# Optimization experiments

Measured on AMD Instinct MI355X. Metric: run time of the kernel, lower is better.

## Reference

```python
import jax, jax.numpy as jnp
import numpy as np

DIM = 1024
HID = 512
N_EXPERTS = 16
TOP_K = 4


def setup_inputs() -> dict:
    key = jax.random.key(0)
    ks = jax.random.split(key, 8)
    s = 0.02
    x = jax.random.normal(ks[0], (2, 1024, DIM), dtype=jnp.float32)
    gate_w = jax.random.normal(ks[1], (N_EXPERTS, DIM), dtype=jnp.float32) * s
    # stacked expert weights (nn.Linear stores [out, in]; we keep [E, out, in])
    w1 = jax.random.normal(ks[2], (N_EXPERTS, HID, DIM), dtype=jnp.float32) * s
    w3 = jax.random.normal(ks[3], (N_EXPERTS, HID, DIM), dtype=jnp.float32) * s
    w2 = jax.random.normal(ks[4], (N_EXPERTS, DIM, HID), dtype=jnp.float32) * s
    sw1 = jax.random.normal(ks[5], (HID, DIM), dtype=jnp.float32) * s
    sw3 = jax.random.normal(ks[6], (HID, DIM), dtype=jnp.float32) * s
    sw2 = jax.random.normal(ks[7], (DIM, HID), dtype=jnp.float32) * s
    return {"x": x, "gate_w": gate_w, "w1": w1, "w3": w3, "w2": w2,
            "sw1": sw1, "sw3": sw3, "sw2": sw2}


def reference(x, gate_w, w1, w3, w2, sw1, sw3, sw2):
    bsz, seq_len, dim = x.shape
    xf = x.reshape(-1, dim)                              # [T, d]
    T = xf.shape[0]

    # router: softmax -> top-k -> renormalize
    probs = jax.nn.softmax(xf @ gate_w.T, axis=-1)       # [T, E]
    top_w, top_idx = jax.lax.top_k(probs, TOP_K)         # [T, K]
    top_w = top_w / jnp.sum(top_w, axis=-1, keepdims=True)

    # combine weights as dense [T, E] (zero for unselected experts);
    # weighted dense per-expert compute is mathematically identical to the
    # gather/scatter loop since unselected experts get weight 0.
    rows = jnp.arange(T)[:, None]
    combine = jnp.zeros((T, N_EXPERTS), dtype=xf.dtype).at[rows, top_idx].set(top_w)

    h1 = jnp.einsum('td,ehd->teh', xf, w1)               # [T, E, h]
    h3 = jnp.einsum('td,ehd->teh', xf, w3)
    act = jax.nn.silu(h1) * h3
    eout = jnp.einsum('teh,edh->ted', act, w2)           # [T, E, d]
    moe_out = jnp.einsum('ted,te->td', eout, combine)    # [T, d]

    shared = (jax.nn.silu(xf @ sw1.T) * (xf @ sw3.T)) @ sw2.T
    return (moe_out + shared).reshape(bsz, seq_len, dim)
```

## Files before the change

### kernel.cpp

```cpp
#include <hip/hip_runtime.h>

#define DIM   1024
#define HID   512
#define NEXP  16
#define TOPK  4
#define SLOTS 5
#define PITCH 72
#define TPE   16

typedef unsigned short u16;
typedef unsigned int   u32;
typedef short bf16x8 __attribute__((ext_vector_type(8)));
typedef float f32x4  __attribute__((ext_vector_type(4)));

__device__ __forceinline__ float bf2f(u16 u) {
    union { u32 i; float f; } v; v.i = ((u32)u) << 16; return v.f;
}
__device__ __forceinline__ u16 f2bf(float f) {
    union { float f; u32 i; } v; v.f = f;
    u32 lsb = (v.i >> 16) & 1u;
    v.i += 0x7fffu + lsb;
    return (u16)(v.i >> 16);
}
__device__ __forceinline__ uint4 pack8(float4 a, float4 b) {
    uint4 r;
    r.x = (u32)f2bf(a.x) | ((u32)f2bf(a.y) << 16);
    r.y = (u32)f2bf(a.z) | ((u32)f2bf(a.w) << 16);
    r.z = (u32)f2bf(b.x) | ((u32)f2bf(b.y) << 16);
    r.w = (u32)f2bf(b.z) | ((u32)f2bf(b.w) << 16);
    return r;
}

#define CW ((size_t)NEXP * HID * DIM / 8)
#define CS ((size_t)HID * DIM / 8)
#define SEG_B0 (CW)
#define SEG_B1 (SEG_B0 + CS)
#define SEG_B2 (SEG_B1 + CW)
#define SEG_B3 (SEG_B2 + CS)
#define SEG_B4 (SEG_B3 + CW)
#define SEG_B5 (SEG_B4 + CS)

__global__ __launch_bounds__(256) void moe_prep(
    const float* __restrict__ x,    const float* __restrict__ gate,
    const float* __restrict__ w1,   const float* __restrict__ w3,
    const float* __restrict__ w2,   const float* __restrict__ sw1,
    const float* __restrict__ sw3,  const float* __restrict__ sw2,
    u16* __restrict__ dst,
    int* __restrict__ counts, u32* __restrict__ pairs,
    float* __restrict__ wslot, int T)
{
    const int blk = blockIdx.x;
    const int tid = threadIdx.x;
    if (blk >= T) {
        const size_t base = (size_t)(blk - T) * 512 + tid;
        const size_t totC = SEG_B5 + ((size_t)T << 7);
#pragma unroll
        for (int h = 0; h < 2; ++h) {
            const size_t c = base + (size_t)h * 256;
            if (c >= totC) break;
            const float* src; size_t loc;
            if      (c < SEG_B0) { src = w1;  loc = c; }
            else if (c < SEG_B1) { src = sw1; loc = c - SEG_B0; }
            else if (c < SEG_B2) { src = w3;  loc = c - SEG_B1; }
            else if (c < SEG_B3) { src = sw3; loc = c - SEG_B2; }
            else if (c < SEG_B4) { src = w2;  loc = c - SEG_B3; }
            else if (c < SEG_B5) { src = sw2; loc = c - SEG_B4; }
            else                 { src = x;   loc = c - SEG_B5; }
            float4 a = ((const float4*)src)[loc * 2];
            float4 b = ((const float4*)src)[loc * 2 + 1];
            ((uint4*)dst)[c] = pack8(a, b);
        }
        return;
    }
    const int t    = blk;
    const int lane = tid & 63;
    const int wv   = tid >> 6;
    const float* xrow = x + (size_t)t * DIM;
    float xr[16];
#pragma unroll
    for (int j = 0; j < 16; ++j) xr[j] = xrow[lane + 64 * j];

    __shared__ float slog[NEXP];
#pragma unroll
    for (int i = 0; i < 4; ++i) {
        const int e = wv * 4 + i;
        const float* g = gate + (size_t)e * DIM;
        float s = 0.f;
#pragma unroll
        for (int j = 0; j < 16; ++j) s += xr[j] * g[lane + 64 * j];
#pragma unroll
        for (int off = 32; off > 0; off >>= 1) s += __shfl_xor(s, off);
        if (lane == 0) slog[e] = s;
    }
    __syncthreads();
    if (wv != 0) return;

    float v[NEXP];
#pragma unroll
    for (int e = 0; e < NEXP; ++e) v[e] = slog[e];
    int idx[TOPK]; float lv[TOPK];
#pragma unroll
    for (int r = 0; r < TOPK; ++r) {
        int be = 0; float bv = v[0];
        for (int e = 1; e < NEXP; ++e) { if (v[e] > bv) { bv = v[e]; be = e; } }
        idx[r] = be; lv[r] = bv; v[be] = -3.0e38f;
    }
    float wk[TOPK]; float wsum = 0.f;
#pragma unroll
    for (int r = 0; r < TOPK; ++r) { wk[r] = __expf(lv[r] - lv[0]); wsum += wk[r]; }
#pragma unroll
    for (int r = 0; r < TOPK; ++r) wk[r] /= wsum;

    if (lane < TOPK) {
        int e = idx[lane];
        int slot = atomicAdd(&counts[e], 1);
        if (slot < T) pairs[(size_t)e * T + slot] = ((u32)t << 3) | (u32)lane;
        wslot[t * SLOTS + lane] = wk[lane];
    } else if (lane == TOPK) {
        pairs[(size_t)NEXP * T + t] = ((u32)t << 3) | 4u;
        wslot[t * SLOTS + 4] = 1.0f;
    }
}

__global__ __launch_bounds__(256) void moe_gemm1(
    const u16* __restrict__ xb,
    const u16* __restrict__ w1c, const u16* __restrict__ w3c,
    const u32* __restrict__ pairs, const int* __restrict__ counts,
    u16* __restrict__ act, int T)
{
    const int ytile = blockIdx.y;
    const int e     = ytile % (NEXP + 1);
    const int ti    = ytile / (NEXP + 1);
    const int r0    = ti << 7;
    const int n0    = blockIdx.x * 128;
    const int cnt = (e == NEXP) ? T : min(max(counts[e], 0), T);
    if (r0 >= cnt) return;
    const int nv = min(128, cnt - r0);

    const u16* W1 = w1c + (size_t)e * HID * DIM;
    const u16* W3 = w3c + (size_t)e * HID * DIM;

    __shared__ __align__(16) u16 sA [128 * PITCH];
    __shared__ __align__(16) u16 sB1[128 * PITCH];
    __shared__ __align__(16) u16 sB3[128 * PITCH];
    __shared__ u32 sEnt[128];

    const int tid = threadIdx.x;
    if (tid < 128) {
        u32 ent = (tid < nv) ? pairs[(size_t)e * T + r0 + tid] : 0u;
        u32 tk = ent >> 3, sl = ent & 7u;
        if (tk >= (u32)T) tk = 0;
        if (sl >= SLOTS)  sl = 0;
        sEnt[tid] = (tk << 3) | sl;
    }
    __syncthreads();

    const int ar = tid >> 1;
    const int ac = (tid & 1) * 32;
    const u16* xrow  = xb + (size_t)(sEnt[ar] >> 3) * DIM;
    const u16* b1row = W1 + (size_t)(n0 + ar) * DIM;
    const u16* b3row = W3 + (size_t)(n0 + ar) * DIM;

    const int wv   = tid >> 6;
    const int lane = tid & 63;
    const int l15  = lane & 15;
    const int kq   = (lane >> 4) * 8;
    const int m0   = (wv & 1) * 64;
    const int nc0  = (wv >> 1) * 64;

    f32x4 acc1[4][4], acc3[4][4];
#pragma unroll
    for (int i = 0; i < 4; ++i)
#pragma unroll
        for (int j = 0; j < 4; ++j) { acc1[i][j] = (f32x4){0,0,0,0}; acc3[i][j] = (f32x4){0,0,0,0}; }

    for (int kt = 0; kt < DIM; kt += 64) {
        __syncthreads();
        *(uint4*)&sA [ar*PITCH + ac]      = *(const uint4*)&xrow [kt + ac];
        *(uint4*)&sA [ar*PITCH + ac +  8] = *(const uint4*)&xrow [kt + ac +  8];
        *(uint4*)&sA [ar*PITCH + ac + 16] = *(const uint4*)&xrow [kt + ac + 16];
        *(uint4*)&sA [ar*PITCH + ac + 24] = *(const uint4*)&xrow [kt + ac + 24];
        *(uint4*)&sB1[ar*PITCH + ac]      = *(const uint4*)&b1row[kt + ac];
        *(uint4*)&sB1[ar*PITCH + ac +  8] = *(const uint4*)&b1row[kt + ac +  8];
        *(uint4*)&sB1[ar*PITCH + ac + 16] = *(const uint4*)&b1row[kt + ac + 16];
        *(uint4*)&sB1[ar*PITCH + ac + 24] = *(const uint4*)&b1row[kt + ac + 24];
        *(uint4*)&sB3[ar*PITCH + ac]      = *(const uint4*)&b3row[kt + ac];
        *(uint4*)&sB3[ar*PITCH + ac +  8] = *(const uint4*)&b3row[kt + ac +  8];
        *(uint4*)&sB3[ar*PITCH + ac + 16] = *(const uint4*)&b3row[kt + ac + 16];
        *(uint4*)&sB3[ar*PITCH + ac + 24] = *(const uint4*)&b3row[kt + ac + 24];
        __syncthreads();
#pragma unroll
        for (int ks = 0; ks < 64; ks += 32) {
            bf16x8 af[4], b1f[4], b3f[4];
#pragma unroll
            for (int mf = 0; mf < 4; ++mf)
                af[mf] = *(const bf16x8*)&sA[(m0 + mf*16 + l15)*PITCH + ks + kq];
#pragma unroll
            for (int nf = 0; nf < 4; ++nf) {
                b1f[nf] = *(const bf16x8*)&sB1[(nc0 + nf*16 + l15)*PITCH + ks + kq];
                b3f[nf] = *(const bf16x8*)&sB3[(nc0 + nf*16 + l15)*PITCH + ks + kq];
            }
#pragma unroll
            for (int mf = 0; mf < 4; ++mf)
#pragma unroll
                for (int nf = 0; nf < 4; ++nf) {
                    acc1[mf][nf] = __builtin_amdgcn_mfma_f32_16x16x32_bf16(af[mf], b1f[nf], acc1[mf][nf], 0, 0, 0);
                    acc3[mf][nf] = __builtin_amdgcn_mfma_f32_16x16x32_bf16(af[mf], b3f[nf], acc3[mf][nf], 0, 0, 0);
                }
        }
    }
#pragma unroll
    for (int mf = 0; mf < 4; ++mf)
#pragma unroll
    for (int nf = 0; nf < 4; ++nf)
#pragma unroll
    for (int r = 0; r < 4; ++r) {
        int ml = m0 + mf*16 + (lane >> 4)*4 + r;
        if (ml < nv) {
            float h1 = acc1[mf][nf][r], h3 = acc3[mf][nf][r];
            float a = (h1 / (1.f + __expf(-h1))) * h3;
            u32 ent = sEnt[ml];
            size_t sidx = (size_t)(ent >> 3) * SLOTS + (ent & 7u);
            act[sidx * HID + n0 + nc0 + nf*16 + l15] = f2bf(a);
        }
    }
}

__global__ __launch_bounds__(256) void moe_gemm2(
    const u16* __restrict__ act, const u16* __restrict__ w2c,
    const u32* __restrict__ pairs, const float* __restrict__ wslot,
    const int* __restrict__ counts,
    u16* __restrict__ eout, float* __restrict__ out, int useEout, int T)
{
    const int ytile = blockIdx.y;
    const int e     = ytile % (NEXP + 1);
    const int ti    = ytile / (NEXP + 1);
    const int r0    = ti << 7;
    const int n0    = blockIdx.x * 128;
    const int cnt = (e == NEXP) ? T : min(max(counts[e], 0), T);
    if (r0 >= cnt) return;
    const int nv = min(128, cnt - r0);

    const u16* W2 = w2c + (size_t)e * DIM * HID;

    __shared__ __align__(16) u16 sA[128 * PITCH];
    __shared__ __align__(16) u16 sB[128 * PITCH];
    __shared__ u32 sEnt[128];

    const int tid = threadIdx.x;
    if (tid < 128) {
        u32 ent = (tid < nv) ? pairs[(size_t)e * T + r0 + tid] : 0u;
        u32 tk = ent >> 3, sl = ent & 7u;
        if (tk >= (u32)T) tk = 0;
        if (sl >= SLOTS)  sl = 0;
        sEnt[tid] = (tk << 3) | sl;
    }
    __syncthreads();

    const int ar = tid >> 1;
    const int ac = (tid & 1) * 32;
    const u32 entA = sEnt[ar];
    const u16* arow = act + ((size_t)(entA >> 3) * SLOTS + (entA & 7u)) * HID;
    const u16* brow = W2 + (size_t)(n0 + ar) * HID;

    const int wv   = tid >> 6;
    const int lane = tid & 63;
    const int l15  = lane & 15;
    const int kq   = (lane >> 4) * 8;
    const int m0   = (wv & 1) * 64;
    const int nc0  = (wv >> 1) * 64;

    f32x4 acc[4][4];
#pragma unroll
    for (int i = 0; i < 4; ++i)
#pragma unroll
        for (int j = 0; j < 4; ++j) acc[i][j] = (f32x4){0,0,0,0};

    for (int kt = 0; kt < HID; kt += 64) {
        __syncthreads();
        *(uint4*)&sA[ar*PITCH + ac]      = *(const uint4*)&arow[kt + ac];
        *(uint4*)&sA[ar*PITCH + ac +  8] = *(const uint4*)&arow[kt + ac +  8];
        *(uint4*)&sA[ar*PITCH + ac + 16] = *(const uint4*)&arow[kt + ac + 16];
        *(uint4*)&sA[ar*PITCH + ac + 24] = *(const uint4*)&arow[kt + ac + 24];
        *(uint4*)&sB[ar*PITCH + ac]      = *(const uint4*)&brow[kt + ac];
        *(uint4*)&sB[ar*PITCH + ac +  8] = *(const uint4*)&brow[kt + ac +  8];
        *(uint4*)&sB[ar*PITCH + ac + 16] = *(const uint4*)&brow[kt + ac + 16];
        *(uint4*)&sB[ar*PITCH + ac + 24] = *(const uint4*)&brow[kt + ac + 24];
        __syncthreads();
#pragma unroll
        for (int ks = 0; ks < 64; ks += 32) {
            bf16x8 af[4], bf[4];
#pragma unroll
            for (int mf = 0; mf < 4; ++mf)
                af[mf] = *(const bf16x8*)&sA[(m0 + mf*16 + l15)*PITCH + ks + kq];
#pragma unroll
            for (int nf = 0; nf < 4; ++nf)
                bf[nf] = *(const bf16x8*)&sB[(nc0 + nf*16 + l15)*PITCH + ks + kq];
#pragma unroll
            for (int mf = 0; mf < 4; ++mf)
#pragma unroll
                for (int nf = 0; nf < 4; ++nf)
                    acc[mf][nf] = __builtin_amdgcn_mfma_f32_16x16x32_bf16(af[mf], bf[nf], acc[mf][nf], 0, 0, 0);
        }
    }
#pragma unroll
    for (int mf = 0; mf < 4; ++mf)
#pragma unroll
    for (int nf = 0; nf < 4; ++nf)
#pragma unroll
    for (int r = 0; r < 4; ++r) {
        int ml = m0 + mf*16 + (lane >> 4)*4 + r;
        if (ml < nv) {
            u32 ent = sEnt[ml];
            u32 tk = ent >> 3;
            float cw = wslot[tk * SLOTS + (ent & 7u)];
            int col = n0 + nc0 + nf*16 + l15;
            float v = cw * acc[mf][nf][r];
            if (useEout) {
                size_t sidx = (size_t)tk * SLOTS + (ent & 7u);
                eout[sidx * DIM + col] = f2bf(v);
            } else {
                atomicAdd(&out[(size_t)tk * DIM + col], v);
            }
        }
    }
}

__global__ __launch_bounds__(256) void moe_combine(
    const u16* __restrict__ eout, float* __restrict__ out, int n4)
{
    int i = blockIdx.x * 256 + threadIdx.x;
    if (i >= n4) return;
    int o4 = i * 4;
    int t = o4 >> 10;
    int col = o4 & 1023;
    float a0 = 0.f, a1 = 0.f, a2 = 0.f, a3 = 0.f;
#pragma unroll
    for (int s = 0; s < SLOTS; ++s) {
        const u16* row = eout + ((size_t)t * SLOTS + s) * DIM + col;
        ushort4 u = *(const ushort4*)row;
        a0 += bf2f(u.x); a1 += bf2f(u.y); a2 += bf2f(u.z); a3 += bf2f(u.w);
    }
    float4* op = (float4*)(out + (size_t)t * DIM + col);
    *op = (float4){a0, a1, a2, a3};
}

extern "C" void kernel_launch(void* const* d_in, const int* in_sizes, int n_in,
                              void* d_out, int out_size, void* d_ws, size_t ws_size,
                              hipStream_t stream)
{
    (void)n_in; (void)out_size;
    const float* x    = (const float*)d_in[0];
    const float* gate = (const float*)d_in[1];
    const float* w1   = (const float*)d_in[2];
    const float* w3   = (const float*)d_in[3];
    const float* w2   = (const float*)d_in[4];
    const float* sw1  = (const float*)d_in[5];
    const float* sw3  = (const float*)d_in[6];
    const float* sw2  = (const float*)d_in[7];
    float* out = (float*)d_out;
    const int T = in_sizes[0] / DIM;

    char* w = (char*)d_ws;
    int*  counts = (int*)(w);
    size_t off = 4096;
    u32*   pairs = (u32*)(w + off);  off += (size_t)(NEXP + 1) * T * 4;
    float* wslot = (float*)(w + off); off += (size_t)T * SLOTS * 4;
    off = (off + 255) & ~(size_t)255;
    u16*   actb  = (u16*)(w + off);  off += (size_t)T * SLOTS * HID * 2;
    off = (off + 255) & ~(size_t)255;
    u16*   cvtb  = (u16*)(w + off);
    const size_t xChunks = (size_t)T * DIM / 8;
    const size_t cvtChunks = SEG_B5 + xChunks;
    off += cvtChunks * 8 * 2;
    off = (off + 255) & ~(size_t)255;
    u16*   eoutb = (u16*)(w + off);
    const size_t needEout = off + (size_t)T * SLOTS * DIM * 2;

    u16* W1c = cvtb;
    u16* W3c = cvtb + SEG_B1 * 8;
    u16* W2c = cvtb + SEG_B3 * 8;
    u16* xb  = cvtb + SEG_B5 * 8;

    const int useEout = (ws_size >= needEout) ? 1 : 0;

    hipMemsetAsync(w, 0, 256, stream);
    if (!useEout)
        hipMemsetAsync(out, 0, (size_t)T * DIM * sizeof(float), stream);

    const int nCvt = (int)((cvtChunks + 511) / 512);
    moe_prep<<<T + nCvt, 256, 0, stream>>>(
        x, gate, w1, w3, w2, sw1, sw3, sw2, cvtb, counts, pairs, wslot, T);

    moe_gemm1<<<dim3(HID / 128, (NEXP + 1) * TPE), 256, 0, stream>>>(
        xb, W1c, W3c, pairs, counts, actb, T);
    moe_gemm2<<<dim3(DIM / 128, (NEXP + 1) * TPE), 256, 0, stream>>>(
        actb, W2c, pairs, wslot, counts, eoutb, out, useEout, T);
    if (useEout)
        moe_combine<<<(T * DIM / 4 + 255) / 256, 256, 0, stream>>>(
            eoutb, out, T * DIM / 4);
}
```

Measured before the change: 285.5 us.

## Shrink grouped GEMM tiles to 64 rows and use nontemporal loads in weight conversion

```diff
diff --git a/kernel.cpp b/kernel.cpp
--- a/kernel.cpp
+++ b/kernel.cpp
@@ -6,12 +6,14 @@
 #define TOPK  4
 #define SLOTS 5
 #define PITCH 72
-#define TPE   16
+#define TPE1  32
 
 typedef unsigned short u16;
 typedef unsigned int   u32;
 typedef short bf16x8 __attribute__((ext_vector_type(8)));
 typedef float f32x4  __attribute__((ext_vector_type(4)));
+typedef float f32x4v __attribute__((ext_vector_type(4)));
+typedef unsigned int u32x4v __attribute__((ext_vector_type(4)));
 
 __device__ __forceinline__ float bf2f(u16 u) {
     union { u32 i; float f; } v; v.i = ((u32)u) << 16; return v.f;
@@ -22,8 +24,8 @@
     v.i += 0x7fffu + lsb;
     return (u16)(v.i >> 16);
 }
-__device__ __forceinline__ uint4 pack8(float4 a, float4 b) {
-    uint4 r;
+__device__ __forceinline__ u32x4v pack8v(f32x4v a, f32x4v b) {
+    u32x4v r;
     r.x = (u32)f2bf(a.x) | ((u32)f2bf(a.y) << 16);
     r.y = (u32)f2bf(a.z) | ((u32)f2bf(a.w) << 16);
     r.z = (u32)f2bf(b.x) | ((u32)f2bf(b.y) << 16);
@@ -66,9 +68,9 @@
             else if (c < SEG_B4) { src = w2;  loc = c - SEG_B3; }
             else if (c < SEG_B5) { src = sw2; loc = c - SEG_B4; }
             else                 { src = x;   loc = c - SEG_B5; }
-            float4 a = ((const float4*)src)[loc * 2];
-            float4 b = ((const float4*)src)[loc * 2 + 1];
-            ((uint4*)dst)[c] = pack8(a, b);
+            f32x4v a = __builtin_nontemporal_load((const f32x4v*)src + loc * 2);
+            f32x4v b = __builtin_nontemporal_load((const f32x4v*)src + loc * 2 + 1);
+            __builtin_nontemporal_store(pack8v(a, b), (u32x4v*)dst + c);
         }
         return;
     }
@@ -131,22 +133,22 @@
     const int ytile = blockIdx.y;
     const int e     = ytile % (NEXP + 1);
     const int ti    = ytile / (NEXP + 1);
-    const int r0    = ti << 7;
-    const int n0    = blockIdx.x * 128;
+    const int r0    = ti << 6;
+    const int n0    = blockIdx.x * 64;
     const int cnt = (e == NEXP) ? T : min(max(counts[e], 0), T);
     if (r0 >= cnt) return;
-    const int nv = min(128, cnt - r0);
+    const int nv = min(64, cnt - r0);
 
     const u16* W1 = w1c + (size_t)e * HID * DIM;
     const u16* W3 = w3c + (size_t)e * HID * DIM;
 
-    __shared__ __align__(16) u16 sA [128 * PITCH];
-    __shared__ __align__(16) u16 sB1[128 * PITCH];
-    __shared__ __align__(16) u16 sB3[128 * PITCH];
-    __shared__ u32 sEnt[128];
+    __shared__ __align__(16) u16 sA [64 * PITCH];
+    __shared__ __align__(16) u16 sB1[64 * PITCH];
+    __shared__ __align__(16) u16 sB3[64 * PITCH];
+    __shared__ u32 sEnt[64];
 
     const int tid = threadIdx.x;
-    if (tid < 128) {
+    if (tid < 64) {
         u32 ent = (tid < nv) ? pairs[(size_t)e * T + r0 + tid] : 0u;
         u32 tk = ent >> 3, sl = ent & 7u;
         if (tk >= (u32)T) tk = 0;
@@ -155,8 +157,8 @@
     }
     __syncthreads();
 
-    const int ar = tid >> 1;
-    const int ac = (tid & 1) * 32;
+    const int ar = tid >> 2;
+    const int ac = (tid & 3) * 16;
     const u16* xrow  = xb + (size_t)(sEnt[ar] >> 3) * DIM;
     const u16* b1row = W1 + (size_t)(n0 + ar) * DIM;
     const u16* b3row = W3 + (size_t)(n0 + ar) * DIM;
@@ -165,54 +167,48 @@
     const int lane = tid & 63;
     const int l15  = lane & 15;
     const int kq   = (lane >> 4) * 8;
-    const int m0   = (wv & 1) * 64;
-    const int nc0  = (wv >> 1) * 64;
-
-    f32x4 acc1[4][4], acc3[4][4];
-#pragma unroll
-    for (int i = 0; i < 4; ++i)
-#pragma unroll
-        for (int j = 0; j < 4; ++j) { acc1[i][j] = (f32x4){0,0,0,0}; acc3[i][j] = (f32x4){0,0,0,0}; }
+    const int m0   = (wv & 1) * 32;
+    const int nc0  = (wv >> 1) * 32;
+
+    f32x4 acc1[2][2], acc3[2][2];
+#pragma unroll
+    for (int i = 0; i < 2; ++i)
+#pragma unroll
+        for (int j = 0; j < 2; ++j) { acc1[i][j] = (f32x4){0,0,0,0}; acc3[i][j] = (f32x4){0,0,0,0}; }
 
     for (int kt = 0; kt < DIM; kt += 64) {
         __syncthreads();
         *(uint4*)&sA [ar*PITCH + ac]      = *(const uint4*)&xrow [kt + ac];
-        *(uint4*)&sA [ar*PITCH + ac +  8] = *(const uint4*)&xrow [kt + ac +  8];
-        *(uint4*)&sA [ar*PITCH + ac + 16] = *(const uint4*)&xrow [kt + ac + 16];
-        *(uint4*)&sA [ar*PITCH + ac + 24] = *(const uint4*)&xrow [kt + ac + 24];
+        *(uint4*)&sA [ar*PITCH + ac + 8]  = *(const uint4*)&xrow [kt + ac + 8];
         *(uint4*)&sB1[ar*PITCH + ac]      = *(const uint4*)&b1row[kt + ac];
-        *(uint4*)&sB1[ar*PITCH + ac +  8] = *(const uint4*)&b1row[kt + ac +  8];
-        *(uint4*)&sB1[ar*PITCH + ac + 16] = *(const uint4*)&b1row[kt + ac + 16];
-        *(uint4*)&sB1[ar*PITCH + ac + 24] = *(const uint4*)&b1row[kt + ac + 24];
+        *(uint4*)&sB1[ar*PITCH + ac + 8]  = *(const uint4*)&b1row[kt + ac + 8];
         *(uint4*)&sB3[ar*PITCH + ac]      = *(const uint4*)&b3row[kt + ac];
-        *(uint4*)&sB3[ar*PITCH + ac +  8] = *(const uint4*)&b3row[kt + ac +  8];
-        *(uint4*)&sB3[ar*PITCH + ac + 16] = *(const uint4*)&b3row[kt + ac + 16];
-        *(uint4*)&sB3[ar*PITCH + ac + 24] = *(const uint4*)&b3row[kt + ac + 24];
+        *(uint4*)&sB3[ar*PITCH + ac + 8]  = *(const uint4*)&b3row[kt + ac + 8];
         __syncthreads();
 #pragma unroll
         for (int ks = 0; ks < 64; ks += 32) {
-            bf16x8 af[4], b1f[4], b3f[4];
-#pragma unroll
-            for (int mf = 0; mf < 4; ++mf)
+            bf16x8 af[2], b1f[2], b3f[2];
+#pragma unroll
+            for (int mf = 0; mf < 2; ++mf)
                 af[mf] = *(const bf16x8*)&sA[(m0 + mf*16 + l15)*PITCH + ks + kq];
 #pragma unroll
-            for (int nf = 0; nf < 4; ++nf) {
+            for (int nf = 0; nf < 2; ++nf) {
                 b1f[nf] = *(const bf16x8*)&sB1[(nc0 + nf*16 + l15)*PITCH + ks + kq];
                 b3f[nf] = *(const bf16x8*)&sB3[(nc0 + nf*16 + l15)*PITCH + ks + kq];
             }
 #pragma unroll
-            for (int mf = 0; mf < 4; ++mf)
-#pragma unroll
-                for (int nf = 0; nf < 4; ++nf) {
+            for (int mf = 0; mf < 2; ++mf)
+#pragma unroll
+                for (int nf = 0; nf < 2; ++nf) {
                     acc1[mf][nf] = __builtin_amdgcn_mfma_f32_16x16x32_bf16(af[mf], b1f[nf], acc1[mf][nf], 0, 0, 0);
                     acc3[mf][nf] = __builtin_amdgcn_mfma_f32_16x16x32_bf16(af[mf], b3f[nf], acc3[mf][nf], 0, 0, 0);
                 }
         }
     }
 #pragma unroll
-    for (int mf = 0; mf < 4; ++mf)
-#pragma unroll
-    for (int nf = 0; nf < 4; ++nf)
+    for (int mf = 0; mf < 2; ++mf)
+#pragma unroll
+    for (int nf = 0; nf < 2; ++nf)
 #pragma unroll
     for (int r = 0; r < 4; ++r) {
         int ml = m0 + mf*16 + (lane >> 4)*4 + r;
@@ -235,20 +231,20 @@
     const int ytile = blockIdx.y;
     const int e     = ytile % (NEXP + 1);
     const int ti    = ytile / (NEXP + 1);
-    const int r0    = ti << 7;
+    const int r0    = ti << 6;
     const int n0    = blockIdx.x * 128;
     const int cnt = (e == NEXP) ? T : min(max(counts[e], 0), T);
     if (r0 >= cnt) return;
-    const int nv = min(128, cnt - r0);
+    const int nv = min(64, cnt - r0);
 
     const u16* W2 = w2c + (size_t)e * DIM * HID;
 
-    __shared__ __align__(16) u16 sA[128 * PITCH];
+    __shared__ __align__(16) u16 sA[ 64 * PITCH];
     __shared__ __align__(16) u16 sB[128 * PITCH];
-    __shared__ u32 sEnt[128];
+    __shared__ u32 sEnt[64];
 
     const int tid = threadIdx.x;
-    if (tid < 128) {
+    if (tid < 64) {
         u32 ent = (tid < nv) ? pairs[(size_t)e * T + r0 + tid] : 0u;
         u32 tk = ent >> 3, sl = ent & 7u;
         if (tk >= (u32)T) tk = 0;
@@ -257,54 +253,54 @@
     }
     __syncthreads();
 
-    const int ar = tid >> 1;
-    const int ac = (tid & 1) * 32;
+    const int ar = tid >> 2;
+    const int ac = (tid & 3) * 16;
     const u32 entA = sEnt[ar];
     const u16* arow = act + ((size_t)(entA >> 3) * SLOTS + (entA & 7u)) * HID;
-    const u16* brow = W2 + (size_t)(n0 + ar) * HID;
+    const int br = tid >> 1;
+    const int bc = (tid & 1) * 32;
+    const u16* brow = W2 + (size_t)(n0 + br) * HID;
 
     const int wv   = tid >> 6;
     const int lane = tid & 63;
     const int l15  = lane & 15;
     const int kq   = (lane >> 4) * 8;
-    const int m0   = (wv & 1) * 64;
+    const int m0   = (wv & 1) * 32;
     const int nc0  = (wv >> 1) * 64;
 
-    f32x4 acc[4][4];
-#pragma unroll
-    for (int i = 0; i < 4; ++i)
+    f32x4 acc[2][4];
+#pragma unroll
+    for (int i = 0; i < 2; ++i)
 #pragma unroll
         for (int j = 0; j < 4; ++j) acc[i][j] = (f32x4){0,0,0,0};
 
     for (int kt = 0; kt < HID; kt += 64) {
         __syncthreads();
         *(uint4*)&sA[ar*PITCH + ac]      = *(const uint4*)&arow[kt + ac];
-        *(uint4*)&sA[ar*PITCH + ac +  8] = *(const uint4*)&arow[kt + ac +  8];
-        *(uint4*)&sA[ar*PITCH + ac + 16] = *(const uint4*)&arow[kt + ac + 16];
-        *(uint4*)&sA[ar*PITCH + ac + 24] = *(const uint4*)&arow[kt + ac + 24];
-        *(uint4*)&sB[ar*PITCH + ac]      = *(const uint4*)&brow[kt + ac];
-        *(uint4*)&sB[ar*PITCH + ac +  8] = *(const uint4*)&brow[kt + ac +  8];
-        *(uint4*)&sB[ar*PITCH + ac + 16] = *(const uint4*)&brow[kt + ac + 16];
-        *(uint4*)&sB[ar*PITCH + ac + 24] = *(const uint4*)&brow[kt + ac + 24];
+        *(uint4*)&sA[ar*PITCH + ac + 8]  = *(const uint4*)&arow[kt + ac + 8];
+        *(uint4*)&sB[br*PITCH + bc]      = *(const uint4*)&brow[kt + bc];
+        *(uint4*)&sB[br*PITCH + bc +  8] = *(const uint4*)&brow[kt + bc +  8];
+        *(uint4*)&sB[br*PITCH + bc + 16] = *(const uint4*)&brow[kt + bc + 16];
+        *(uint4*)&sB[br*PITCH + bc + 24] = *(const uint4*)&brow[kt + bc + 24];
         __syncthreads();
 #pragma unroll
         for (int ks = 0; ks < 64; ks += 32) {
-            bf16x8 af[4], bf[4];
-#pragma unroll
-            for (int mf = 0; mf < 4; ++mf)
+            bf16x8 af[2], bf[4];
+#pragma unroll
+            for (int mf = 0; mf < 2; ++mf)
                 af[mf] = *(const bf16x8*)&sA[(m0 + mf*16 + l15)*PITCH + ks + kq];
 #pragma unroll
             for (int nf = 0; nf < 4; ++nf)
                 bf[nf] = *(const bf16x8*)&sB[(nc0 + nf*16 + l15)*PITCH + ks + kq];
 #pragma unroll
-            for (int mf = 0; mf < 4; ++mf)
+            for (int mf = 0; mf < 2; ++mf)
 #pragma unroll
                 for (int nf = 0; nf < 4; ++nf)
                     acc[mf][nf] = __builtin_amdgcn_mfma_f32_16x16x32_bf16(af[mf], bf[nf], acc[mf][nf], 0, 0, 0);
         }
     }
 #pragma unroll
-    for (int mf = 0; mf < 4; ++mf)
+    for (int mf = 0; mf < 2; ++mf)
 #pragma unroll
     for (int nf = 0; nf < 4; ++nf)
 #pragma unroll
@@ -392,9 +388,9 @@
     moe_prep<<<T + nCvt, 256, 0, stream>>>(
         x, gate, w1, w3, w2, sw1, sw3, sw2, cvtb, counts, pairs, wslot, T);
 
-    moe_gemm1<<<dim3(HID / 128, (NEXP + 1) * TPE), 256, 0, stream>>>(
+    moe_gemm1<<<dim3(HID / 64, (NEXP + 1) * TPE1), 256, 0, stream>>>(
         xb, W1c, W3c, pairs, counts, actb, T);
-    moe_gemm2<<<dim3(DIM / 128, (NEXP + 1) * TPE), 256, 0, stream>>>(
+    moe_gemm2<<<dim3(DIM / 128, (NEXP + 1) * TPE1), 256, 0, stream>>>(
         actb, W2c, pairs, wslot, counts, eoutb, out, useEout, T);
     if (useEout)
         moe_combine<<<(T * DIM / 4 + 255) / 256, 256, 0, stream>>>(
```

Result: faster. 264.4 us (-7.4%).
